# Optimization experiments

Hardware: AMD Instinct MI355X
Metric: run time of the kernel (lower is better)

## Reference

```python
import jax, jax.numpy as jnp
import numpy as np

C = 384          # hardcoded input dim in Head
H = 6            # num_heads
D = 64           # head_size (H*D == C)

def setup_inputs() -> dict:
    key = jax.random.key(0)
    ks = jax.random.split(key, 6)
    x = jax.random.normal(ks[0], (4, 2048, C), dtype=jnp.float32)
    # per-head projection weights stacked: [H, C, D]
    s = 1.0 / np.sqrt(C)
    Wq = jax.random.uniform(ks[1], (H, C, D), minval=-s, maxval=s, dtype=jnp.float32)
    Wk = jax.random.uniform(ks[2], (H, C, D), minval=-s, maxval=s, dtype=jnp.float32)
    Wv = jax.random.uniform(ks[3], (H, C, D), minval=-s, maxval=s, dtype=jnp.float32)
    sp = 1.0 / np.sqrt(H * D)
    Wo = jax.random.uniform(ks[4], (H * D, H * D), minval=-sp, maxval=sp, dtype=jnp.float32)
    bo = jax.random.uniform(ks[5], (H * D,), minval=-sp, maxval=sp, dtype=jnp.float32)
    return {"x": x, "Wq": Wq, "Wk": Wk, "Wv": Wv, "Wo": Wo, "bo": bo}

def reference(x, Wq, Wk, Wv, Wo, bo):
    B, T, _ = x.shape
    # per-head projections (batched over heads instead of a Python loop)
    q = jnp.einsum('btc,hcd->bhtd', x, Wq)
    k = jnp.einsum('btc,hcd->bhtd', x, Wk)
    v = jnp.einsum('btc,hcd->bhtd', x, Wv)
    scale = 1.0 / jnp.sqrt(jnp.asarray(D, dtype=x.dtype))
    scores = jnp.einsum('bhtd,bhsd->bhts', q, k) * scale  # [B,H,T,T]
    attn = jax.nn.softmax(scores, axis=-1)                # no causal mask in source
    out = jnp.einsum('bhts,bhsd->bhtd', attn, v)          # [B,H,T,D]
    # concat heads: [B,T,H*D] (head order matches torch.cat over heads)
    out = out.transpose(0, 2, 1, 3).reshape(B, T, H * D)
    return out @ Wo + bo
```

## Files before the change

kernel.cpp:

```cpp
#include <hip/hip_runtime.h>

typedef unsigned short u16;
typedef float  f32x4  __attribute__((ext_vector_type(4)));
typedef float  f32x16 __attribute__((ext_vector_type(16)));
typedef short  s16x8  __attribute__((ext_vector_type(8)));
typedef unsigned int u32x2 __attribute__((ext_vector_type(2)));
typedef unsigned int u32x4 __attribute__((ext_vector_type(4)));

union U8 { u32x4 u; u32x2 u2[2]; s16x8 s; unsigned int uw[4]; };

__device__ __forceinline__ u16 f2bs(float f) {
    union { float f; unsigned int u; } x; x.f = f;
    return (u16)((x.u + 0x7FFFu + ((x.u >> 16) & 1u)) >> 16);
}

__device__ __forceinline__ unsigned int cvtpk(float a, float b) {
    unsigned int r;
    asm("v_cvt_pk_bf16_f32 %0, %1, %2" : "=v"(r) : "v"(a), "v"(b));
    return r;
}

#if __has_builtin(__builtin_amdgcn_exp2f)
#define EXP2(v) __builtin_amdgcn_exp2f(v)
#else
#define EXP2(v) exp2f(v)
#endif

__device__ __forceinline__ f32x4 mfma16(s16x8 a, s16x8 b, f32x4 c) {
    return __builtin_amdgcn_mfma_f32_16x16x32_bf16(a, b, c, 0, 0, 0);
}
__device__ __forceinline__ f32x16 mfma32(s16x8 a, s16x8 b, f32x16 c) {
    return __builtin_amdgcn_mfma_f32_32x32x16_bf16(a, b, c, 0, 0, 0);
}

typedef __attribute__((address_space(3))) unsigned int lds_u32;
typedef const __attribute__((address_space(1))) unsigned int glb_u32;
__device__ __forceinline__ void gl16(const u16* g, u16* l) {
    __builtin_amdgcn_global_load_lds((glb_u32*)g, (lds_u32*)l, 16, 0, 0);
}

__global__ __launch_bounds__(256) void pack_w2(const float* __restrict__ Wq,
                                               const float* __restrict__ Wk,
                                               const float* __restrict__ Wv,
                                               const float* __restrict__ Wo,
                                               u16* __restrict__ Wt) {
    __shared__ float tile[64][65];
    const int bid = blockIdx.x, tid = threadIdx.x;
    const float* src; u16* dst; int src_ld, sr0, sc0;
    if (bid < 108) {
        int tensor = bid / 36, rem = bid % 36, h = rem / 6, ct = rem % 6;
        const float* W = (tensor == 0) ? Wq : (tensor == 1) ? Wk : Wv;
        src = W + h * 24576; src_ld = 64; sr0 = ct * 64; sc0 = 0;
        dst = Wt + tensor * 147456 + h * 24576;
    } else {
        int rem = bid - 108, et = rem / 6, ft = rem % 6;
        src = Wo; src_ld = 384; sr0 = ft * 64; sc0 = et * 64;
        dst = Wt + 3 * 147456;
    }
    const int r = tid >> 2, cb = (tid & 3) * 16;
    const float* sp = src + (size_t)(sr0 + r) * src_ld + sc0 + cb;
    #pragma unroll
    for (int j = 0; j < 4; ++j)
        *(f32x4*)&tile[r][cb + j * 4] = *(const f32x4*)(sp + j * 4);
    __syncthreads();
    struct alignas(16) OV { u16 v[16]; } ov;
    #pragma unroll
    for (int j = 0; j < 16; ++j) ov.v[j] = f2bs(tile[cb + j][r]);
    u16* dp = dst + (size_t)(sc0 + r) * 384 + sr0 + cb;
    *(u32x4*)dp       = *(u32x4*)&ov.v[0];
    *(u32x4*)(dp + 8) = *(u32x4*)&ov.v[8];
}

__global__ __launch_bounds__(256) void convert_x(const float* __restrict__ x, u16* __restrict__ xb) {
    const int i = (blockIdx.x * 256 + threadIdx.x) * 8;
    f32x4 a = *(const f32x4*)(x + i);
    f32x4 b = *(const f32x4*)(x + i + 4);
    U8 o;
    #pragma unroll
    for (int j = 0; j < 4; ++j) { o.s[j] = (short)f2bs(a[j]); o.s[4 + j] = (short)f2bs(b[j]); }
    *(u32x4*)(xb + i) = o.u;
}

__global__ __launch_bounds__(256) void proj2(const u16* __restrict__ xb,
                                             const u16* __restrict__ Wt,
                                             u16* __restrict__ Qb,
                                             u16* __restrict__ Kb,
                                             u16* __restrict__ Vb) {
    __shared__ u16 As[2][128 * 32];
    __shared__ u16 Bs[2][128 * 32];
    const int tid = threadIdx.x, w = tid >> 6, lane = tid & 63;
    const int lr = lane & 15, lg = lane >> 4;
    const int wr = w >> 1, wc = w & 1;
    const int mt = blockIdx.x, nt = blockIdx.y;
    const int m0 = mt * 128, n0 = nt * 128;

    const int c0 = w * 2 * 64 + lane;
    const int ar0 = c0 >> 2, acc0 = c0 & 3;
    const int c1 = c0 + 64;
    const int ar1 = c1 >> 2, acc1 = c1 & 3;
    const u16* gA0 = xb + (size_t)(m0 + ar0) * 384 + acc0 * 8;
    const u16* gA1 = xb + (size_t)(m0 + ar1) * 384 + acc1 * 8;
    const u16* gB0 = Wt + (size_t)(n0 + ar0) * 384 + acc0 * 8;
    const u16* gB1 = Wt + (size_t)(n0 + ar1) * 384 + acc1 * 8;

    f32x4 acc[4][4];
    #pragma unroll
    for (int i = 0; i < 4; ++i)
        #pragma unroll
        for (int j = 0; j < 4; ++j) acc[i][j] = f32x4{0.f, 0.f, 0.f, 0.f};

    gl16(gA0, &As[0][(w * 2 + 0) * 512]);
    gl16(gA1, &As[0][(w * 2 + 1) * 512]);
    gl16(gB0, &Bs[0][(w * 2 + 0) * 512]);
    gl16(gB1, &Bs[0][(w * 2 + 1) * 512]);
    __syncthreads();

    for (int kt = 0; kt < 12; ++kt) {
        const int buf = kt & 1;
        if (kt < 11) {
            const int ko = (kt + 1) * 32;
            gl16(gA0 + ko, &As[buf ^ 1][(w * 2 + 0) * 512]);
            gl16(gA1 + ko, &As[buf ^ 1][(w * 2 + 1) * 512]);
            gl16(gB0 + ko, &Bs[buf ^ 1][(w * 2 + 0) * 512]);
            gl16(gB1 + ko, &Bs[buf ^ 1][(w * 2 + 1) * 512]);
        }
        U8 af[4], bf[4];
        #pragma unroll
        for (int f = 0; f < 4; ++f) {
            af[f].u = *(const u32x4*)&As[buf][(wr * 64 + f * 16 + lr) * 32 + lg * 8];
            bf[f].u = *(const u32x4*)&Bs[buf][(wc * 64 + f * 16 + lr) * 32 + lg * 8];
        }
        #pragma unroll
        for (int mf = 0; mf < 4; ++mf)
            #pragma unroll
            for (int nf = 0; nf < 4; ++nf)
                acc[mf][nf] = mfma16(af[mf].s, bf[nf].s, acc[mf][nf]);
        __syncthreads();
    }

    const int tensor = nt / 3;
    u16* dst = (tensor == 0) ? Qb : (tensor == 1) ? Kb : Vb;
    const float scl = (tensor == 0) ? 0.18033688011112042f : 1.0f;
    const int head_base = (nt % 3) * 2 + wc;
    #pragma unroll
    for (int mf = 0; mf < 4; ++mf)
        #pragma unroll
        for (int nf = 0; nf < 4; ++nf)
            #pragma unroll
            for (int r = 0; r < 4; ++r) {
                int m = m0 + wr * 64 + mf * 16 + lg * 4 + r;
                int b = m >> 11, t = m & 2047;
                int d = nf * 16 + lr;
                dst[((size_t)(b * 6 + head_base) * 2048 + t) * 64 + d] = f2bs(acc[mf][nf][r] * scl);
            }
}

__global__ __launch_bounds__(256) void transpose_v(const u16* __restrict__ Vb,
                                                   u16* __restrict__ Vt) {
    __shared__ u16 tile[64][72];
    const int bh = blockIdx.y, t0 = blockIdx.x * 64;
    const int tid = threadIdx.x;
    const int r = tid >> 2, c0 = (tid & 3) * 16;
    const u16* src = Vb + ((size_t)bh * 2048 + t0 + r) * 64 + c0;
    u32x4 a  = *(const u32x4*)(src);
    u32x4 b2 = *(const u32x4*)(src + 8);
    *(u32x4*)&tile[r][c0]     = a;
    *(u32x4*)&tile[r][c0 + 8] = b2;
    __syncthreads();
    struct alignas(16) OutV { u16 v[16]; } ov;
    #pragma unroll
    for (int j = 0; j < 4; ++j) {
        ov.v[j]      = tile[c0 + j][r];
        ov.v[4 + j]  = tile[c0 + 8 + j][r];
        ov.v[8 + j]  = tile[c0 + 4 + j][r];
        ov.v[12 + j] = tile[c0 + 12 + j][r];
    }
    u16* dst = Vt + ((size_t)bh * 64 + r) * 2048 + t0 + c0;
    *(u32x4*)dst       = *(u32x4*)&ov.v[0];
    *(u32x4*)(dst + 8) = *(u32x4*)&ov.v[8];
}

__global__ __launch_bounds__(256, 3) void attn6(const u16* __restrict__ Qb,
                                                const u16* __restrict__ Kb,
                                                const u16* __restrict__ Vt,
                                                u16* __restrict__ AO) {
    __shared__ float ms[8448];
    const int tid = threadIdx.x, wv = tid >> 6, lane = tid & 63;
    const int q = lane & 31, hi = lane >> 5;
    const int bh = blockIdx.x, qt = blockIdx.y;
    const int b = bh / 6, h = bh - b * 6;
    const int qbase = qt * 64;

    const u16* qp = Qb + ((size_t)bh * 2048 + qbase + q) * 64 + hi * 8;
    U8 bq[2][4];
    #pragma unroll
    for (int qs = 0; qs < 2; ++qs)
        #pragma unroll
        for (int m = 0; m < 4; ++m)
            bq[qs][m].u = *(const u32x4*)(qp + qs * 2048 + m * 16);

    const u16* kb_l = Kb + (size_t)bh * 131072 + (size_t)wv * 32768 + q * 64 + hi * 8;
    const u16* vb_l = Vt + (size_t)bh * 131072 + (size_t)q * 2048 + wv * 512 + hi * 8;

    f32x16 acc[2][2];
    #pragma unroll
    for (int i = 0; i < 2; ++i)
        #pragma unroll
        for (int j = 0; j < 2; ++j)
            #pragma unroll
            for (int r = 0; r < 16; ++r) acc[i][j][r] = 0.f;
    float rs0 = 0.f, rs1 = 0.f;

    #pragma unroll 2
    for (int it = 0; it < 16; ++it) {
        const u16* kp = kb_l + it * 2048;
        U8 kf[4];
        #pragma unroll
        for (int m = 0; m < 4; ++m) kf[m].u = *(const u32x4*)(kp + m * 16);

        f32x16 S0, S1;
        #pragma unroll
        for (int r = 0; r < 16; ++r) { S0[r] = 0.f; S1[r] = 0.f; }
        #pragma unroll
        for (int m = 0; m < 4; ++m) S0 = mfma32(kf[m].s, bq[0][m].s, S0);
        #pragma unroll
        for (int m = 0; m < 4; ++m) S1 = mfma32(kf[m].s, bq[1][m].s, S1);

        float p0[16], p1[16];
        #pragma unroll
        for (int r = 0; r < 16; ++r) { p0[r] = EXP2(S0[r]); p1[r] = EXP2(S1[r]); }
        #pragma unroll
        for (int r = 0; r < 16; ++r) { rs0 += p0[r]; rs1 += p1[r]; }

        U8 pa[2][2];
        #pragma unroll
        for (int i = 0; i < 4; ++i) {
            pa[0][0].uw[i] = cvtpk(p0[2 * i],     p0[2 * i + 1]);
            pa[0][1].uw[i] = cvtpk(p0[8 + 2 * i], p0[9 + 2 * i]);
            pa[1][0].uw[i] = cvtpk(p1[2 * i],     p1[2 * i + 1]);
            pa[1][1].uw[i] = cvtpk(p1[8 + 2 * i], p1[9 + 2 * i]);
        }

        const int ko = it * 32;
        #pragma unroll
        for (int dt2 = 0; dt2 < 2; ++dt2) {
            U8 bv0, bv1;
            bv0.u = *(const u32x4*)(vb_l + dt2 * 65536 + ko);
            bv1.u = *(const u32x4*)(vb_l + dt2 * 65536 + ko + 16);
            acc[0][dt2] = mfma32(pa[0][0].s, bv0.s, acc[0][dt2]);
            acc[0][dt2] = mfma32(pa[0][1].s, bv1.s, acc[0][dt2]);
            acc[1][dt2] = mfma32(pa[1][0].s, bv0.s, acc[1][dt2]);
            acc[1][dt2] = mfma32(pa[1][1].s, bv1.s, acc[1][dt2]);
        }
    }

    rs0 += __shfl_xor(rs0, 32, 64);
    rs1 += __shfl_xor(rs1, 32, 64);

    float* r0 = ms;
    float* r1 = ms + 4224;

    if (wv == 1) {
        #pragma unroll
        for (int qs = 0; qs < 2; ++qs)
            #pragma unroll
            for (int dt2 = 0; dt2 < 2; ++dt2)
                #pragma unroll
                for (int r = 0; r < 16; ++r) {
                    int row = qs * 32 + (r & 3) + 8 * (r >> 2) + 4 * hi;
                    r0[row * 64 + dt2 * 32 + q] = acc[qs][dt2][r];
                }
        r0[4096 + lane] = rs0; r0[4160 + lane] = rs1;
    } else if (wv == 3) {
        #pragma unroll
        for (int qs = 0; qs < 2; ++qs)
            #pragma unroll
            for (int dt2 = 0; dt2 < 2; ++dt2)
                #pragma unroll
                for (int r = 0; r < 16; ++r) {
                    int row = qs * 32 + (r & 3) + 8 * (r >> 2) + 4 * hi;
                    r1[row * 64 + dt2 * 32 + q] = acc[qs][dt2][r];
                }
        r1[4096 + lane] = rs0; r1[4160 + lane] = rs1;
    }
    __syncthreads();
    if (wv == 0) {
        #pragma unroll
        for (int qs = 0; qs < 2; ++qs)
            #pragma unroll
            for (int dt2 = 0; dt2 < 2; ++dt2)
                #pragma unroll
                for (int r = 0; r < 16; ++r) {
                    int row = qs * 32 + (r & 3) + 8 * (r >> 2) + 4 * hi;
                    acc[qs][dt2][r] += r0[row * 64 + dt2 * 32 + q];
                }
        rs0 += r0[4096 + lane]; rs1 += r0[4160 + lane];
    } else if (wv == 2) {
        #pragma unroll
        for (int qs = 0; qs < 2; ++qs)
            #pragma unroll
            for (int dt2 = 0; dt2 < 2; ++dt2)
                #pragma unroll
                for (int r = 0; r < 16; ++r) {
                    int row = qs * 32 + (r & 3) + 8 * (r >> 2) + 4 * hi;
                    acc[qs][dt2][r] += r1[row * 64 + dt2 * 32 + q];
                }
        rs0 += r1[4096 + lane]; rs1 += r1[4160 + lane];
    }
    __syncthreads();
    if (wv == 2) {
        #pragma unroll
        for (int qs = 0; qs < 2; ++qs)
            #pragma unroll
            for (int dt2 = 0; dt2 < 2; ++dt2)
                #pragma unroll
                for (int r = 0; r < 16; ++r) {
                    int row = qs * 32 + (r & 3) + 8 * (r >> 2) + 4 * hi;
                    r0[row * 64 + dt2 * 32 + q] = acc[qs][dt2][r];
                }
        r0[4096 + lane] = rs0; r0[4160 + lane] = rs1;
    }
    __syncthreads();
    if (wv == 0) {
        #pragma unroll
        for (int qs = 0; qs < 2; ++qs)
            #pragma unroll
            for (int dt2 = 0; dt2 < 2; ++dt2)
                #pragma unroll
                for (int r = 0; r < 16; ++r) {
                    int row = qs * 32 + (r & 3) + 8 * (r >> 2) + 4 * hi;
                    acc[qs][dt2][r] += r0[row * 64 + dt2 * 32 + q];
                }
        rs0 += r0[4096 + lane]; rs1 += r0[4160 + lane];

        const float inv0 = 1.0f / rs0;
        const float inv1 = 1.0f / rs1;
        const size_t aobase = ((size_t)b * 2048 + qbase) * 384 + h * 64;
        #pragma unroll
        for (int qs = 0; qs < 2; ++qs)
            #pragma unroll
            for (int r = 0; r < 16; ++r) {
                const int crow = (r & 3) + 8 * (r >> 2) + 4 * hi;
                const int qrow = qs * 32 + crow;
                float vinv = __shfl(qs == 0 ? inv0 : inv1, crow, 64);
                #pragma unroll
                for (int dt2 = 0; dt2 < 2; ++dt2)
                    AO[aobase + (size_t)qrow * 384 + dt2 * 32 + q] = f2bs(acc[qs][dt2][r] * vinv);
            }
    }
}

__global__ __launch_bounds__(256) void outproj2(const u16* __restrict__ AO,
                                                const u16* __restrict__ Wot,
                                                const float* __restrict__ bo,
                                                float* __restrict__ out) {
    __shared__ u16 As[2][64 * 32];
    __shared__ u16 Bs[2][64 * 32];
    const int tid = threadIdx.x, w = tid >> 6, lane = tid & 63;
    const int lr = lane & 15, lg = lane >> 4;
    const int wr = w >> 1, wc = w & 1;
    const int mt = blockIdx.x, nt = blockIdx.y;
    const int m0 = mt * 64, n0 = nt * 64;

    const int c0 = w * 64 + lane;
    const int ar0 = c0 >> 2, cc0 = c0 & 3;
    const u16* gA = AO  + (size_t)(m0 + ar0) * 384 + cc0 * 8;
    const u16* gB = Wot + (size_t)(n0 + ar0) * 384 + cc0 * 8;

    f32x4 acc[2][2];
    #pragma unroll
    for (int i = 0; i < 2; ++i)
        #pragma unroll
        for (int j = 0; j < 2; ++j) acc[i][j] = f32x4{0.f, 0.f, 0.f, 0.f};

    gl16(gA, &As[0][w * 512]);
    gl16(gB, &Bs[0][w * 512]);
    __syncthreads();

    for (int kt = 0; kt < 12; ++kt) {
        const int buf = kt & 1;
        if (kt < 11) {
            const int ko = (kt + 1) * 32;
            gl16(gA + ko, &As[buf ^ 1][w * 512]);
            gl16(gB + ko, &Bs[buf ^ 1][w * 512]);
        }
        U8 af[2], bf[2];
        #pragma unroll
        for (int f = 0; f < 2; ++f) {
            af[f].u = *(const u32x4*)&As[buf][(wr * 32 + f * 16 + lr) * 32 + lg * 8];
            bf[f].u = *(const u32x4*)&Bs[buf][(wc * 32 + f * 16 + lr) * 32 + lg * 8];
        }
        #pragma unroll
        for (int mf = 0; mf < 2; ++mf)
            #pragma unroll
            for (int nf = 0; nf < 2; ++nf)
                acc[mf][nf] = mfma16(af[mf].s, bf[nf].s, acc[mf][nf]);
        __syncthreads();
    }

    #pragma unroll
    for (int mf = 0; mf < 2; ++mf)
        #pragma unroll
        for (int nf = 0; nf < 2; ++nf) {
            int col = n0 + wc * 32 + nf * 16 + lr;
            float bias = bo[col];
            #pragma unroll
            for (int r = 0; r < 4; ++r) {
                int m = m0 + wr * 32 + mf * 16 + lg * 4 + r;
                out[(size_t)m * 384 + col] = acc[mf][nf][r] + bias;
            }
        }
}

extern "C" void kernel_launch(void* const* d_in, const int* in_sizes, int n_in,
                              void* d_out, int out_size, void* d_ws, size_t ws_size,
                              hipStream_t stream) {
    const float* x  = (const float*)d_in[0];
    const float* Wq = (const float*)d_in[1];
    const float* Wk = (const float*)d_in[2];
    const float* Wv = (const float*)d_in[3];
    const float* Wo = (const float*)d_in[4];
    const float* bo = (const float*)d_in[5];
    float* out = (float*)d_out;
    char* ws = (char*)d_ws;

    u16* Wt  = (u16*)(ws);
    u16* Wot = (u16*)(ws + 884736);
    u16* xb  = (u16*)(ws + 1179648);
    u16* Qb  = (u16*)(ws + 7471104);
    u16* Kb  = (u16*)(ws + 13762560);
    u16* Vb  = (u16*)(ws + 20054016);
    u16* Vt  = (u16*)(ws + 26345472);
    u16* AO  = (u16*)(ws + 1179648);

    pack_w2<<<144, 256, 0, stream>>>(Wq, Wk, Wv, Wo, Wt);
    convert_x<<<1536, 256, 0, stream>>>(x, xb);
    proj2<<<dim3(64, 9), 256, 0, stream>>>(xb, Wt, Qb, Kb, Vb);
    transpose_v<<<dim3(32, 24), 256, 0, stream>>>(Vb, Vt);
    attn6<<<dim3(24, 32), 256, 0, stream>>>(Qb, Kb, Vt, AO);
    outproj2<<<dim3(128, 6), 256, 0, stream>>>(AO, Wot, bo, out);
}
```

Before: 154.5 us.

## Stage K/V tiles through double-buffered LDS with async global-to-LDS loads in attention

The attention kernel now prefetches per-wave K and V tiles into swizzled shared memory using global_load_lds, double-buffered, with explicit vmcnt waits and scheduling barriers. Before this, each step loaded fragments directly from global memory into registers. The goal is to overlap memory latency with MFMA/exp work and to avoid LDS bank conflicts through XOR swizzling. In exchange it uses 64KB of LDS per block and lowers the occupancy target from 3 to 2 blocks, and it depends on hand-placed waitcnt correctness.

```diff
diff --git a/kernel.cpp b/kernel.cpp
--- a/kernel.cpp
+++ b/kernel.cpp
@@ -38,6 +38,11 @@
 __device__ __forceinline__ void gl16(const u16* g, u16* l) {
     __builtin_amdgcn_global_load_lds((glb_u32*)g, (lds_u32*)l, 16, 0, 0);
 }
+
+#define VMW8  asm volatile("s_waitcnt vmcnt(8)" ::: "memory")
+#define VMW0  asm volatile("s_waitcnt vmcnt(0)" ::: "memory")
+#define LKW0  asm volatile("s_waitcnt lgkmcnt(0)" ::: "memory")
+#define SB0   __builtin_amdgcn_sched_barrier(0)
 
 __global__ __launch_bounds__(256) void pack_w2(const float* __restrict__ Wq,
                                                const float* __restrict__ Wk,
@@ -180,11 +185,74 @@
     *(u32x4*)(dst + 8) = *(u32x4*)&ov.v[8];
 }
 
-__global__ __launch_bounds__(256, 3) void attn6(const u16* __restrict__ Qb,
+__device__ __forceinline__ void cstep(const char* base, const int koff[4], const int voff[4],
+                                      const U8 bq[2][4], f32x16 acc[2][2],
+                                      float& rs0, float& rs1) {
+    U8 ak0, ak1, ak2, ak3, bv0, bv1, bv2, bv3;
+    ak0.u = *(const u32x4*)(base + koff[0]);
+    ak1.u = *(const u32x4*)(base + koff[1]);
+    ak2.u = *(const u32x4*)(base + koff[2]);
+    ak3.u = *(const u32x4*)(base + koff[3]);
+    bv0.u = *(const u32x4*)(base + voff[0]);
+    bv1.u = *(const u32x4*)(base + voff[1]);
+    bv2.u = *(const u32x4*)(base + voff[2]);
+    bv3.u = *(const u32x4*)(base + voff[3]);
+
+    f32x16 S0, S1;
+    #pragma unroll
+    for (int r = 0; r < 16; ++r) { S0[r] = 0.f; S1[r] = 0.f; }
+    S0 = mfma32(ak0.s, bq[0][0].s, S0);
+    S0 = mfma32(ak1.s, bq[0][1].s, S0);
+    S0 = mfma32(ak2.s, bq[0][2].s, S0);
+    S0 = mfma32(ak3.s, bq[0][3].s, S0);
+    S1 = mfma32(ak0.s, bq[1][0].s, S1);
+    S1 = mfma32(ak1.s, bq[1][1].s, S1);
+    S1 = mfma32(ak2.s, bq[1][2].s, S1);
+    S1 = mfma32(ak3.s, bq[1][3].s, S1);
+
+    float p0[16], p1[16];
+    #pragma unroll
+    for (int r = 0; r < 16; ++r) { p0[r] = EXP2(S0[r]); p1[r] = EXP2(S1[r]); }
+    #pragma unroll
+    for (int r = 0; r < 16; ++r) { rs0 += p0[r]; rs1 += p1[r]; }
+
+    U8 pa[2][2];
+    #pragma unroll
+    for (int i = 0; i < 4; ++i) {
+        pa[0][0].uw[i] = cvtpk(p0[2 * i],     p0[2 * i + 1]);
+        pa[0][1].uw[i] = cvtpk(p0[8 + 2 * i], p0[9 + 2 * i]);
+        pa[1][0].uw[i] = cvtpk(p1[2 * i],     p1[2 * i + 1]);
+        pa[1][1].uw[i] = cvtpk(p1[8 + 2 * i], p1[9 + 2 * i]);
+    }
+
+    acc[0][0] = mfma32(pa[0][0].s, bv0.s, acc[0][0]);
+    acc[0][0] = mfma32(pa[0][1].s, bv1.s, acc[0][0]);
+    acc[0][1] = mfma32(pa[0][0].s, bv2.s, acc[0][1]);
+    acc[0][1] = mfma32(pa[0][1].s, bv3.s, acc[0][1]);
+    acc[1][0] = mfma32(pa[1][0].s, bv0.s, acc[1][0]);
+    acc[1][0] = mfma32(pa[1][1].s, bv1.s, acc[1][0]);
+    acc[1][1] = mfma32(pa[1][0].s, bv2.s, acc[1][1]);
+    acc[1][1] = mfma32(pa[1][1].s, bv3.s, acc[1][1]);
+}
+
+__device__ __forceinline__ void stg8(const u16* ksrc0, const u16* vsrc0, int it, u16* kd) {
+    const u16* ks = ksrc0 + it * 2048;
+    gl16(ks,        kd);
+    gl16(ks + 512,  kd + 512);
+    gl16(ks + 1024, kd + 1024);
+    gl16(ks + 1536, kd + 1536);
+    const u16* vs = vsrc0 + it * 32;
+    gl16(vs,         kd + 2048);
+    gl16(vs + 32768, kd + 2560);
+    gl16(vs + 65536, kd + 3072);
+    gl16(vs + 98304, kd + 3584);
+}
+
+__global__ __launch_bounds__(256, 2) void attn8(const u16* __restrict__ Qb,
                                                 const u16* __restrict__ Kb,
                                                 const u16* __restrict__ Vt,
                                                 u16* __restrict__ AO) {
-    __shared__ float ms[8448];
+    __shared__ char smem[65536];
     const int tid = threadIdx.x, wv = tid >> 6, lane = tid & 63;
     const int q = lane & 31, hi = lane >> 5;
     const int bh = blockIdx.x, qt = blockIdx.y;
@@ -199,8 +267,25 @@
         for (int m = 0; m < 4; ++m)
             bq[qs][m].u = *(const u32x4*)(qp + qs * 2048 + m * 16);
 
-    const u16* kb_l = Kb + (size_t)bh * 131072 + (size_t)wv * 32768 + q * 64 + hi * 8;
-    const u16* vb_l = Vt + (size_t)bh * 131072 + (size_t)q * 2048 + wv * 512 + hi * 8;
+    const int l8 = lane >> 3, c8 = lane & 7;
+    const u16* ksrc0 = Kb + (size_t)bh * 131072 + (size_t)(wv * 512 + l8) * 64 + (c8 ^ l8) * 8;
+    const int lv4 = lane >> 2, c4 = lane & 3;
+    const u16* vsrc0 = Vt + (size_t)bh * 131072 + (size_t)lv4 * 2048 + wv * 512 + (c4 ^ (lv4 & 3)) * 8;
+
+    u16* kdA = (u16*)(smem + wv * 8192);
+    u16* kdB = (u16*)(smem + 32768 + wv * 8192);
+    const char* cbA = smem;
+    const char* cbB = smem + 32768;
+
+    int koff[4], voff[4];
+    #pragma unroll
+    for (int m = 0; m < 4; ++m)
+        koff[m] = wv * 8192 + q * 128 + (((2 * m + hi) ^ (q & 7)) << 4);
+    #pragma unroll
+    for (int dt2 = 0; dt2 < 2; ++dt2)
+        #pragma unroll
+        for (int kg = 0; kg < 2; ++kg)
+            voff[dt2 * 2 + kg] = wv * 8192 + 4096 + dt2 * 2048 + q * 64 + (((2 * kg + hi) ^ (q & 3)) << 4);
 
     f32x16 acc[2][2];
     #pragma unroll
@@ -211,54 +296,29 @@
             for (int r = 0; r < 16; ++r) acc[i][j][r] = 0.f;
     float rs0 = 0.f, rs1 = 0.f;
 
-    #pragma unroll 2
-    for (int it = 0; it < 16; ++it) {
-        const u16* kp = kb_l + it * 2048;
-        U8 kf[4];
-        #pragma unroll
-        for (int m = 0; m < 4; ++m) kf[m].u = *(const u32x4*)(kp + m * 16);
-
-        f32x16 S0, S1;
-        #pragma unroll
-        for (int r = 0; r < 16; ++r) { S0[r] = 0.f; S1[r] = 0.f; }
-        #pragma unroll
-        for (int m = 0; m < 4; ++m) S0 = mfma32(kf[m].s, bq[0][m].s, S0);
-        #pragma unroll
-        for (int m = 0; m < 4; ++m) S1 = mfma32(kf[m].s, bq[1][m].s, S1);
-
-        float p0[16], p1[16];
-        #pragma unroll
-        for (int r = 0; r < 16; ++r) { p0[r] = EXP2(S0[r]); p1[r] = EXP2(S1[r]); }
-        #pragma unroll
-        for (int r = 0; r < 16; ++r) { rs0 += p0[r]; rs1 += p1[r]; }
-
-        U8 pa[2][2];
-        #pragma unroll
-        for (int i = 0; i < 4; ++i) {
-            pa[0][0].uw[i] = cvtpk(p0[2 * i],     p0[2 * i + 1]);
-            pa[0][1].uw[i] = cvtpk(p0[8 + 2 * i], p0[9 + 2 * i]);
-            pa[1][0].uw[i] = cvtpk(p1[2 * i],     p1[2 * i + 1]);
-            pa[1][1].uw[i] = cvtpk(p1[8 + 2 * i], p1[9 + 2 * i]);
-        }
-
-        const int ko = it * 32;
-        #pragma unroll
-        for (int dt2 = 0; dt2 < 2; ++dt2) {
-            U8 bv0, bv1;
-            bv0.u = *(const u32x4*)(vb_l + dt2 * 65536 + ko);
-            bv1.u = *(const u32x4*)(vb_l + dt2 * 65536 + ko + 16);
-            acc[0][dt2] = mfma32(pa[0][0].s, bv0.s, acc[0][dt2]);
-            acc[0][dt2] = mfma32(pa[0][1].s, bv1.s, acc[0][dt2]);
-            acc[1][dt2] = mfma32(pa[1][0].s, bv0.s, acc[1][dt2]);
-            acc[1][dt2] = mfma32(pa[1][1].s, bv1.s, acc[1][dt2]);
-        }
-    }
+    stg8(ksrc0, vsrc0, 0, kdA);
+    stg8(ksrc0, vsrc0, 1, kdB);
+
+    for (int it2 = 0; it2 < 7; ++it2) {
+        VMW8; SB0;
+        cstep(cbA, koff, voff, bq, acc, rs0, rs1);
+        LKW0;
+        stg8(ksrc0, vsrc0, 2 * it2 + 2, kdA);
+        VMW8; SB0;
+        cstep(cbB, koff, voff, bq, acc, rs0, rs1);
+        LKW0;
+        stg8(ksrc0, vsrc0, 2 * it2 + 3, kdB);
+    }
+    VMW8; SB0; cstep(cbA, koff, voff, bq, acc, rs0, rs1);
+    VMW0; SB0; cstep(cbB, koff, voff, bq, acc, rs0, rs1);
 
     rs0 += __shfl_xor(rs0, 32, 64);
     rs1 += __shfl_xor(rs1, 32, 64);
 
-    float* r0 = ms;
-    float* r1 = ms + 4224;
+    __syncthreads();
+
+    float* r0 = (float*)smem;
+    float* r1 = (float*)smem + 4224;
 
     if (wv == 1) {
         #pragma unroll
@@ -437,6 +497,6 @@
     convert_x<<<1536, 256, 0, stream>>>(x, xb);
     proj2<<<dim3(64, 9), 256, 0, stream>>>(xb, Wt, Qb, Kb, Vb);
     transpose_v<<<dim3(32, 24), 256, 0, stream>>>(Vb, Vt);
-    attn6<<<dim3(24, 32), 256, 0, stream>>>(Qb, Kb, Vt, AO);
+    attn8<<<dim3(24, 32), 256, 0, stream>>>(Qb, Kb, Vt, AO);
     outproj2<<<dim3(128, 6), 256, 0, stream>>>(AO, Wot, bo, out);
 }
```

Result: faster. 140.1 us (-9.4%).
